# Optimization experiments

Measured on AMD Instinct MI355X. Metric: run time of the kernel, lower is better.

## Reference

```python
import jax, jax.numpy as jnp
import numpy as np

N = 65536       # tokens (voxels)
C = 128         # dim
H = 4           # num_heads
HD = C // H     # head_dim = 32
NUM_WIN = 1024  # number of windows


def setup_inputs() -> dict:
    key = jax.random.key(0)
    k1, k2, k3, k4 = jax.random.split(key, 4)
    x = jax.random.normal(k1, (N, C), dtype=jnp.float32)
    w_qkv = jax.random.normal(k2, (3 * C, C), dtype=jnp.float32) * 0.02
    w_proj = jax.random.normal(k3, (C, C), dtype=jnp.float32) * 0.02
    b_proj = jnp.zeros((C,), dtype=jnp.float32)
    batch_win_inds = jnp.sort(jax.random.randint(k4, (N,), 0, NUM_WIN)).astype(jnp.int32)
    counts = jax.ops.segment_sum(jnp.ones((N,), jnp.int32), batch_win_inds, num_segments=NUM_WIN)
    offsets = jnp.concatenate([jnp.zeros((1,), jnp.int32), jnp.cumsum(counts)]).astype(jnp.int32)
    return {"x": x, "w_qkv": w_qkv, "w_proj": w_proj, "b_proj": b_proj,
            "batch_win_inds": batch_win_inds, "offsets": offsets, "counts": counts}


def reference(x, w_qkv, w_proj, b_proj, batch_win_inds, offsets, counts):
    # qkv projection (no bias), split, per-head reshape
    qkv = (x @ w_qkv.T).reshape(N, 3, H, HD)          # [N,3,H,HD]
    q = jax.nn.relu(qkv[:, 0])                        # [N,H,HD]
    k = jax.nn.relu(qkv[:, 1])                        # [N,H,HD]
    v = qkv[:, 2]                                     # [N,H,HD]

    kv = jax.ops.segment_sum(
        jnp.einsum('nhc,nhd->nhcd', k, v), batch_win_inds, num_segments=NUM_WIN)
    # per-window key sum s[w,h,c]
    s = jax.ops.segment_sum(k, batch_win_inds, num_segments=NUM_WIN)

    y = jnp.einsum('nhc,nhcd->nhd', q, kv[batch_win_inds])
    z = jnp.sum(s[batch_win_inds] * q, axis=-1, keepdims=True)
    y = y / (z + 1e-6)

    y = y.reshape(N, C)
    return y @ w_proj.T + b_proj
```

## Files before the change

kernel.cpp:

```cpp
#include <hip/hip_runtime.h>

namespace {
constexpr int C     = 128;
constexpr int T     = 64;
constexpr int BLK   = 512;
constexpr int NWIN  = 1024;
constexpr int KVSTR = 40;
constexpr int KTSTR = 72;
constexpr int YNSTR = 136;
constexpr int WSPN  = 131072;
constexpr size_t QN = (size_t)65536 * 128;
}

typedef __attribute__((ext_vector_type(8))) short bf16x8;
typedef __attribute__((ext_vector_type(4))) short sh4;
typedef __attribute__((ext_vector_type(4))) float f32x4;

__device__ __forceinline__ short bf16rne(float f) {
    unsigned u = __float_as_uint(f);
    u += 0x7fffu + ((u >> 16) & 1u);
    return (short)(u >> 16);
}
__device__ __forceinline__ float bf16f(short h) {
    return __uint_as_float(((unsigned)(unsigned short)h) << 16);
}
__device__ __forceinline__ void split1(float f, short& hi, short& lo) {
    hi = bf16rne(f);
    lo = bf16rne(f - bf16f(hi));
}

__global__ void prep_weights(const float* __restrict__ wqkv,
                             const float* __restrict__ wproj,
                             short* __restrict__ wsp) {
    const int i = blockIdx.x * 256 + threadIdx.x;
    const float f = (i < 49152) ? wqkv[i] : wproj[i - 49152];
    short hi, lo;
    split1(f, hi, lo);
    wsp[i] = hi;
    wsp[65536 + i] = lo;
}

__global__ __launch_bounds__(BLK, 2)
void qkv_gemm(const float* __restrict__ x,
              const short* __restrict__ wsp,
              short* __restrict__ qws,
              short* __restrict__ kws,
              short* __restrict__ vws)
{
    __shared__ __align__(16) short xh[64 * YNSTR];
    __shared__ __align__(16) short xl[64 * YNSTR];

    const int tid = threadIdx.x;
    const int wv = tid >> 6, ln = tid & 63;
    const int fr = ln & 15, fg = ln >> 4;
    const int r0 = blockIdx.x * 256;

    bf16x8 Bh[3][4], Bl[3][4];
#pragma unroll
    for (int ni = 0; ni < 3; ++ni)
#pragma unroll
        for (int ksi = 0; ksi < 4; ++ksi) {
            const int idx = ((3 * wv + ni) * 16 + fr) * C + ksi * 32 + fg * 8;
            Bh[ni][ksi] = *(const bf16x8*)(wsp + idx);
            Bl[ni][ksi] = *(const bf16x8*)(wsp + 65536 + idx);
        }

    const int trow = tid >> 3;
    const int toff = (tid & 7) << 4;

    for (int ch = 0; ch < 4; ++ch) {
        const int rbase = r0 + ch * 64;
        if (ch) __syncthreads();

#pragma unroll
        for (int it = 0; it < 2; ++it) {
            const int i = tid + it * BLK;
            const int t = i >> 4, c8 = (i & 15) << 3;
            const float* p = x + (size_t)(rbase + t) * C + c8;
            const float4 a = *(const float4*)p;
            const float4 b = *(const float4*)(p + 4);
            const float f[8] = {a.x, a.y, a.z, a.w, b.x, b.y, b.z, b.w};
            bf16x8 hi, lo;
#pragma unroll
            for (int u = 0; u < 8; ++u) { short h_, l_; split1(f[u], h_, l_); hi[u] = h_; lo[u] = l_; }
            *(bf16x8*)(xh + t * YNSTR + c8) = hi;
            *(bf16x8*)(xl + t * YNSTR + c8) = lo;
        }
        __syncthreads();

        f32x4 acc[3][4];
#pragma unroll
        for (int ni = 0; ni < 3; ++ni)
#pragma unroll
            for (int m = 0; m < 4; ++m) acc[ni][m] = f32x4{0.f, 0.f, 0.f, 0.f};

#pragma unroll
        for (int ksi = 0; ksi < 4; ++ksi) {
            const int koff = ksi * 32 + fg * 8;
            bf16x8 ahi[4], alo[4];
#pragma unroll
            for (int m = 0; m < 4; ++m) {
                const int row = m * 16 + fr;
                ahi[m] = *(const bf16x8*)(xh + row * YNSTR + koff);
                alo[m] = *(const bf16x8*)(xl + row * YNSTR + koff);
            }
#pragma unroll
            for (int ni = 0; ni < 3; ++ni)
#pragma unroll
                for (int m = 0; m < 4; ++m) {
                    acc[ni][m] = __builtin_amdgcn_mfma_f32_16x16x32_bf16(ahi[m], Bh[ni][ksi], acc[ni][m], 0, 0, 0);
                    acc[ni][m] = __builtin_amdgcn_mfma_f32_16x16x32_bf16(ahi[m], Bl[ni][ksi], acc[ni][m], 0, 0, 0);
                    acc[ni][m] = __builtin_amdgcn_mfma_f32_16x16x32_bf16(alo[m], Bh[ni][ksi], acc[ni][m], 0, 0, 0);
                }
        }
        __syncthreads();

#pragma unroll
        for (int ni = 0; ni < 3; ++ni) {
            const int ti = 3 * wv + ni;
            const int p = ti >> 3;
            if (p < 2) {
                short* buf = (p == 0) ? xh : xl;
                const int lc = (ti & 7) * 16 + fr;
#pragma unroll
                for (int m = 0; m < 4; ++m)
#pragma unroll
                    for (int e = 0; e < 4; ++e)
                        buf[(m * 16 + fg * 4 + e) * YNSTR + lc] =
                            bf16rne(fmaxf(acc[ni][m][e], 0.f));
            }
        }
        __syncthreads();
        {
            const bf16x8 q0 = *(const bf16x8*)(xh + trow * YNSTR + toff);
            const bf16x8 q1 = *(const bf16x8*)(xh + trow * YNSTR + toff + 8);
            const bf16x8 k0 = *(const bf16x8*)(xl + trow * YNSTR + toff);
            const bf16x8 k1 = *(const bf16x8*)(xl + trow * YNSTR + toff + 8);
            *(bf16x8*)(qws + (size_t)(rbase + trow) * C + toff)     = q0;
            *(bf16x8*)(qws + (size_t)(rbase + trow) * C + toff + 8) = q1;
            *(bf16x8*)(kws + (size_t)(rbase + trow) * C + toff)     = k0;
            *(bf16x8*)(kws + (size_t)(rbase + trow) * C + toff + 8) = k1;
        }
        __syncthreads();

#pragma unroll
        for (int ni = 0; ni < 3; ++ni) {
            const int ti = 3 * wv + ni;
            if ((ti >> 3) == 2) {
                const int lc = (ti & 7) * 16 + fr;
#pragma unroll
                for (int m = 0; m < 4; ++m)
#pragma unroll
                    for (int e = 0; e < 4; ++e)
                        xh[(m * 16 + fg * 4 + e) * YNSTR + lc] = bf16rne(acc[ni][m][e]);
            }
        }
        __syncthreads();
        {
            const bf16x8 v0 = *(const bf16x8*)(xh + trow * YNSTR + toff);
            const bf16x8 v1 = *(const bf16x8*)(xh + trow * YNSTR + toff + 8);
            *(bf16x8*)(vws + (size_t)(rbase + trow) * C + toff)     = v0;
            *(bf16x8*)(vws + (size_t)(rbase + trow) * C + toff + 8) = v1;
        }
    }
}

__global__ __launch_bounds__(BLK, 2)
void sla_win(const short* __restrict__ qws,
             const short* __restrict__ kws,
             const short* __restrict__ vws,
             const short* __restrict__ wsp,
             const float* __restrict__ bproj,
             const int*   __restrict__ offsets,
             float*       __restrict__ out)
{
    __shared__ __align__(16) short kT[C * KTSTR];
    __shared__ __align__(16) short vT[C * KTSTR];
    __shared__ __align__(16) short yn[T * YNSTR];
    __shared__ __align__(16) short kvs[4 * 32 * KVSTR];
    __shared__ float ss[C];

    const int win = blockIdx.x;
    const int beg = offsets[win];
    const int cnt = offsets[win + 1] - beg;
    if (cnt <= 0) return;
    const int nch = (cnt + T - 1) / T;

    const int tid = threadIdx.x;
    const int wv = tid >> 6, ln = tid & 63;
    const int fr = ln & 15, fg = ln >> 4;
    const int aH = wv >> 1, tw = wv & 1;

    f32x4 kvacc[2] = {{0.f,0.f,0.f,0.f},{0.f,0.f,0.f,0.f}};
    f32x4 sacc = {0.f, 0.f, 0.f, 0.f};
    bf16x8 ones;
#pragma unroll
    for (int u = 0; u < 8; ++u) ones[u] = (short)0x3F80;

    for (int c0 = 0; c0 < nch; ++c0) {
        const int t0 = c0 * T;
        const int tc = (cnt - t0 < T) ? (cnt - t0) : T;

#pragma unroll
        for (int it = 0; it < 2; ++it) {
            const int i = tid + it * BLK;
            const int t = i >> 4, c8 = (i & 15) << 3;
            bf16x8 k8, v8;
#pragma unroll
            for (int u = 0; u < 8; ++u) { k8[u] = 0; v8[u] = 0; }
            if (t < tc) {
                k8 = *(const bf16x8*)(kws + (size_t)(beg + t0 + t) * C + c8);
                v8 = *(const bf16x8*)(vws + (size_t)(beg + t0 + t) * C + c8);
            }
#pragma unroll
            for (int u = 0; u < 8; ++u) {
                const int c = c8 + u;
                const int tt = t ^ (((c >> 3) & 7) << 3);
                kT[c * KTSTR + tt] = k8[u];
                vT[c * KTSTR + tt] = v8[u];
            }
        }
        __syncthreads();

        {
#pragma unroll
            for (int kt = 0; kt < 2; ++kt) {
                const int t8 = kt * 32 + fg * 8;
                const int cch = aH * 32 + tw * 16 + fr;
                const bf16x8 a8 = *(const bf16x8*)(kT + cch * KTSTR + (t8 ^ (((cch >> 3) & 7) << 3)));
                sacc = __builtin_amdgcn_mfma_f32_16x16x32_bf16(a8, ones, sacc, 0, 0, 0);
#pragma unroll
                for (int dt = 0; dt < 2; ++dt) {
                    const int dch = aH * 32 + dt * 16 + fr;
                    const bf16x8 b8 = *(const bf16x8*)(vT + dch * KTSTR + (t8 ^ (((dch >> 3) & 7) << 3)));
                    kvacc[dt] = __builtin_amdgcn_mfma_f32_16x16x32_bf16(a8, b8, kvacc[dt], 0, 0, 0);
                }
            }
        }
        if (c0 + 1 < nch) __syncthreads();
    }

    {
#pragma unroll
        for (int dt = 0; dt < 2; ++dt) {
            const int d = dt * 16 + fr;
#pragma unroll
            for (int e = 0; e < 4; ++e) {
                const int c = tw * 16 + fg * 4 + e;
                kvs[aH * (32 * KVSTR) + d * KVSTR + c] = bf16rne(kvacc[dt][e]);
            }
        }
        if (fr == 0) {
#pragma unroll
            for (int e = 0; e < 4; ++e)
                ss[aH * 32 + tw * 16 + fg * 4 + e] = sacc[e];
        }
    }
    __syncthreads();

    for (int c0 = 0; c0 < nch; ++c0) {
        const int t0 = c0 * T;
        const int tc = (cnt - t0 < T) ? (cnt - t0) : T;

        {
            const int a = wv >> 1, mp = wv & 1;
            bf16x8 bfr[2];
#pragma unroll
            for (int dl = 0; dl < 2; ++dl)
                bfr[dl] = *(const bf16x8*)(kvs + a * (32 * KVSTR) + (dl * 16 + fr) * KVSTR + fg * 8);

            const float4 s0 = *(const float4*)(ss + a * 32 + fg * 8);
            const float4 s1 = *(const float4*)(ss + a * 32 + fg * 8 + 4);

            bf16x8 afr[2];
            float zinv[2];
#pragma unroll
            for (int mi = 0; mi < 2; ++mi) {
                const int row = (mp * 2 + mi) * 16 + fr;
                afr[mi] = *(const bf16x8*)(qws + (size_t)(beg + t0 + row) * C + a * 32 + fg * 8);
                float zp = 0.f;
                zp = fmaf(bf16f(afr[mi][0]), s0.x, zp);
                zp = fmaf(bf16f(afr[mi][1]), s0.y, zp);
                zp = fmaf(bf16f(afr[mi][2]), s0.z, zp);
                zp = fmaf(bf16f(afr[mi][3]), s0.w, zp);
                zp = fmaf(bf16f(afr[mi][4]), s1.x, zp);
                zp = fmaf(bf16f(afr[mi][5]), s1.y, zp);
                zp = fmaf(bf16f(afr[mi][6]), s1.z, zp);
                zp = fmaf(bf16f(afr[mi][7]), s1.w, zp);
                zp += __shfl_xor(zp, 16);
                zp += __shfl_xor(zp, 32);
                zinv[mi] = 1.f / (zp + 1e-6f);
            }
            f32x4 acc[2][2];
#pragma unroll
            for (int mi = 0; mi < 2; ++mi)
#pragma unroll
                for (int dl = 0; dl < 2; ++dl) {
                    acc[mi][dl] = f32x4{0.f, 0.f, 0.f, 0.f};
                    acc[mi][dl] = __builtin_amdgcn_mfma_f32_16x16x32_bf16(afr[mi], bfr[dl], acc[mi][dl], 0, 0, 0);
                }
#pragma unroll
            for (int mi = 0; mi < 2; ++mi)
#pragma unroll
                for (int e = 0; e < 4; ++e) {
                    const float zt = __shfl(zinv[mi], fg * 4 + e);
                    const int t = (mp * 2 + mi) * 16 + fg * 4 + e;
#pragma unroll
                    for (int dl = 0; dl < 2; ++dl) {
                        const int ch = a * 32 + dl * 16 + fr;
                        yn[t * YNSTR + ch] = bf16rne(acc[mi][dl][e] * zt);
                    }
                }
        }
        __syncthreads();

        {
            f32x4 acc[4];
#pragma unroll
            for (int m = 0; m < 4; ++m) acc[m] = f32x4{0.f, 0.f, 0.f, 0.f};
#pragma unroll
            for (int ksi = 0; ksi < 4; ++ksi) {
                const int koff = ksi * 32 + fg * 8;
                bf16x8 a8[4];
#pragma unroll
                for (int m = 0; m < 4; ++m) {
                    const int row = m * 16 + fr;
                    a8[m] = *(const bf16x8*)(yn + row * YNSTR + koff);
                }
                const int idx = (384 + wv * 16 + fr) * C + koff;
                const bf16x8 bhi = *(const bf16x8*)(wsp + idx);
                const bf16x8 blo = *(const bf16x8*)(wsp + 65536 + idx);
#pragma unroll
                for (int m = 0; m < 4; ++m) {
                    acc[m] = __builtin_amdgcn_mfma_f32_16x16x32_bf16(a8[m], bhi, acc[m], 0, 0, 0);
                    acc[m] = __builtin_amdgcn_mfma_f32_16x16x32_bf16(a8[m], blo, acc[m], 0, 0, 0);
                }
            }
            const int ch = wv * 16 + fr;
            const float b = bproj[ch];
#pragma unroll
            for (int m = 0; m < 4; ++m)
#pragma unroll
                for (int e = 0; e < 4; ++e) {
                    const int t = m * 16 + fg * 4 + e;
                    if (t < tc)
                        out[(size_t)(beg + t0 + t) * C + ch] = acc[m][e] + b;
                }
        }
        if (c0 + 1 < nch) __syncthreads();
    }
}

__global__ __launch_bounds__(BLK, 2)
void sla6(const float* __restrict__ x, const float* __restrict__ bproj,
          const int* __restrict__ offsets, const short* __restrict__ wsp,
          short* __restrict__ qws, float* __restrict__ out)
{
    __shared__ __align__(16) short xs_hi[T * C];
    __shared__ __align__(16) short xs_lo[T * C];
    __shared__ __align__(16) short kT[C * T];
    __shared__ __align__(16) short vTy[C * T];
    __shared__ __align__(16) short kvs[4 * 32 * KVSTR];
    __shared__ float ss[C];

    const int win = blockIdx.x;
    const int beg = offsets[win];
    const int cnt = offsets[win + 1] - beg;
    if (cnt <= 0) return;
    const int nch = (cnt + T - 1) / T;

    const int tid = threadIdx.x;
    const int wv = tid >> 6, ln = tid & 63;
    const int fr = ln & 15, fg = ln >> 4;

    auto loadB = [&](int row512, int koff, bf16x8& bhi, bf16x8& blo) {
        const int idx = row512 * C + koff;
        bhi = *(const bf16x8*)(wsp + idx);
        blo = *(const bf16x8*)(wsp + 65536 + idx);
    };
    auto stage = [&](int t0, int tc) {
#pragma unroll
        for (int it = 0; it < 2; ++it) {
            const int i = tid + it * BLK;
            const int t = i >> 4, c8 = (i & 15) << 3;
            float4 a = {0.f, 0.f, 0.f, 0.f}, b = {0.f, 0.f, 0.f, 0.f};
            if (t < tc) {
                const float* p = x + (size_t)(beg + t0 + t) * C + c8;
                a = *(const float4*)p;
                b = *(const float4*)(p + 4);
            }
            const float f[8] = {a.x, a.y, a.z, a.w, b.x, b.y, b.z, b.w};
            bf16x8 hi, lo;
#pragma unroll
            for (int u = 0; u < 8; ++u) { short h_, l_; split1(f[u], h_, l_); hi[u] = h_; lo[u] = l_; }
            const int s = t * C + (c8 ^ ((t & 7) << 3));
            *(bf16x8*)(xs_hi + s) = hi;
            *(bf16x8*)(xs_lo + s) = lo;
        }
    };

    const int aH = wv >> 1, tw = wv & 1;
    f32x4 kvacc[2] = {{0.f,0.f,0.f,0.f},{0.f,0.f,0.f,0.f}};
    f32x4 sacc = {0.f, 0.f, 0.f, 0.f};
    bf16x8 ones;
#pragma unroll
    for (int u = 0; u < 8; ++u) ones[u] = (short)0x3F80;

    for (int c0 = 0; c0 < nch; ++c0) {
        const int t0 = c0 * T;
        const int tc = (cnt - t0 < T) ? (cnt - t0) : T;
        stage(t0, tc);
        __syncthreads();
        sh4 qreg[4];
        {
            f32x4 acc[2][4];
#pragma unroll
            for (int ni = 0; ni < 2; ++ni)
#pragma unroll
                for (int m = 0; m < 4; ++m) acc[ni][m] = f32x4{0.f, 0.f, 0.f, 0.f};
#pragma unroll
            for (int ksi = 0; ksi < 4; ++ksi) {
                const int koff = ksi * 32 + fg * 8;
                bf16x8 ahi[4], alo[4];
#pragma unroll
                for (int m = 0; m < 4; ++m) {
                    const int row = m * 16 + fr;
                    const int s = row * C + (koff ^ ((row & 7) << 3));
                    ahi[m] = *(const bf16x8*)(xs_hi + s);
                    alo[m] = *(const bf16x8*)(xs_lo + s);
                }
#pragma unroll
                for (int ni = 0; ni < 2; ++ni) {
                    bf16x8 bhi, blo;
                    loadB(128 + (2 * wv + ni) * 16 + fr, koff, bhi, blo);
#pragma unroll
                    for (int m = 0; m < 4; ++m) {
                        acc[ni][m] = __builtin_amdgcn_mfma_f32_16x16x32_bf16(ahi[m], bhi, acc[ni][m], 0, 0, 0);
                        acc[ni][m] = __builtin_amdgcn_mfma_f32_16x16x32_bf16(ahi[m], blo, acc[ni][m], 0, 0, 0);
                        acc[ni][m] = __builtin_amdgcn_mfma_f32_16x16x32_bf16(alo[m], bhi, acc[ni][m], 0, 0, 0);
                    }
                }
            }
#pragma unroll
            for (int ni = 0; ni < 2; ++ni) {
                const int nt = 2 * wv + ni;
                const bool isk = (nt < 8);
                const int ch = (isk ? nt : nt - 8) * 16 + fr;
                short* dst = isk ? kT : vTy;
#pragma unroll
                for (int m = 0; m < 4; ++m) {
                    sh4 h4;
#pragma unroll
                    for (int e = 0; e < 4; ++e) {
                        float v = acc[ni][m][e];
                        if (isk) v = fmaxf(v, 0.f);
                        h4[e] = bf16rne(v);
                    }
                    const int tb = m * 16 + fg * 4;
                    *(sh4*)(dst + ch * T + (tb ^ ((ch & 7) << 3))) = h4;
                }
            }
        }
        {
            f32x4 acc[4];
#pragma unroll
            for (int m = 0; m < 4; ++m) acc[m] = f32x4{0.f, 0.f, 0.f, 0.f};
#pragma unroll
            for (int ksi = 0; ksi < 4; ++ksi) {
                const int koff = ksi * 32 + fg * 8;
                bf16x8 ahi[4], alo[4];
#pragma unroll
                for (int m = 0; m < 4; ++m) {
                    const int row = m * 16 + fr;
                    const int s = row * C + (koff ^ ((row & 7) << 3));
                    ahi[m] = *(const bf16x8*)(xs_hi + s);
                    alo[m] = *(const bf16x8*)(xs_lo + s);
                }
                bf16x8 bhi, blo;
                loadB(wv * 16 + fr, koff, bhi, blo);
#pragma unroll
                for (int m = 0; m < 4; ++m) {
                    acc[m] = __builtin_amdgcn_mfma_f32_16x16x32_bf16(ahi[m], bhi, acc[m], 0, 0, 0);
                    acc[m] = __builtin_amdgcn_mfma_f32_16x16x32_bf16(ahi[m], blo, acc[m], 0, 0, 0);
                    acc[m] = __builtin_amdgcn_mfma_f32_16x16x32_bf16(alo[m], bhi, acc[m], 0, 0, 0);
                }
            }
#pragma unroll
            for (int m = 0; m < 4; ++m)
#pragma unroll
                for (int e = 0; e < 4; ++e)
                    qreg[m][e] = bf16rne(fmaxf(acc[m][e], 0.f));
        }
        __syncthreads();
        {
            const int ch = wv * 16 + fr;
            if (nch == 1) {
#pragma unroll
                for (int m = 0; m < 4; ++m)
#pragma unroll
                    for (int e = 0; e < 4; ++e) {
                        const int t = m * 16 + fg * 4 + e;
                        xs_hi[t * C + (ch ^ ((t & 7) << 3))] = qreg[m][e];
                    }
            } else {
#pragma unroll
                for (int m = 0; m < 4; ++m)
#pragma unroll
                    for (int e = 0; e < 4; ++e) {
                        const int t = m * 16 + fg * 4 + e;
                        if (t < tc)
                            qws[(size_t)(beg + t0 + t) * C + ch] = qreg[m][e];
                    }
            }
        }
        {
#pragma unroll
            for (int kt = 0; kt < 2; ++kt) {
                const int t8 = kt * 32 + fg * 8;
                const int cch = aH * 32 + tw * 16 + fr;
                const bf16x8 a8 = *(const bf16x8*)(kT + cch * T + (t8 ^ ((cch & 7) << 3)));
                sacc = __builtin_amdgcn_mfma_f32_16x16x32_bf16(a8, ones, sacc, 0, 0, 0);
#pragma unroll
                for (int dt = 0; dt < 2; ++dt) {
                    const int dch = aH * 32 + dt * 16 + fr;
                    const bf16x8 b8 = *(const bf16x8*)(vTy + dch * T + (t8 ^ ((dch & 7) << 3)));
                    kvacc[dt] = __builtin_amdgcn_mfma_f32_16x16x32_bf16(a8, b8, kvacc[dt], 0, 0, 0);
                }
            }
        }
        if (c0 + 1 < nch) __syncthreads();
    }
    {
#pragma unroll
        for (int dt = 0; dt < 2; ++dt) {
            const int d = dt * 16 + fr;
#pragma unroll
            for (int e = 0; e < 4; ++e) {
                const int c = tw * 16 + fg * 4 + e;
                kvs[aH * (32 * KVSTR) + d * KVSTR + c] = bf16rne(kvacc[dt][e]);
            }
        }
        if (fr == 0) {
#pragma unroll
            for (int e = 0; e < 4; ++e)
                ss[aH * 32 + tw * 16 + fg * 4 + e] = sacc[e];
        }
    }
    __syncthreads();
    for (int c0 = 0; c0 < nch; ++c0) {
        const int t0 = c0 * T;
        const int tc = (cnt - t0 < T) ? (cnt - t0) : T;
        {
            const int a = wv >> 1, mp = wv & 1;
            bf16x8 bfr[2];
#pragma unroll
            for (int dl = 0; dl < 2; ++dl)
                bfr[dl] = *(const bf16x8*)(kvs + a * (32 * KVSTR) + (dl * 16 + fr) * KVSTR + fg * 8);
            const float4 s0 = *(const float4*)(ss + a * 32 + fg * 8);
            const float4 s1 = *(const float4*)(ss + a * 32 + fg * 8 + 4);
            bf16x8 afr[2];
            float zinv[2];
#pragma unroll
            for (int mi = 0; mi < 2; ++mi) {
                const int row = (mp * 2 + mi) * 16 + fr;
                if (nch == 1)
                    afr[mi] = *(const bf16x8*)(xs_hi + row * C + ((a * 32 + fg * 8) ^ ((row & 7) << 3)));
                else
                    afr[mi] = *(const bf16x8*)(qws + (size_t)(beg + t0 + row) * C + a * 32 + fg * 8);
                float zp = 0.f;
                zp = fmaf(bf16f(afr[mi][0]), s0.x, zp);
                zp = fmaf(bf16f(afr[mi][1]), s0.y, zp);
                zp = fmaf(bf16f(afr[mi][2]), s0.z, zp);
                zp = fmaf(bf16f(afr[mi][3]), s0.w, zp);
                zp = fmaf(bf16f(afr[mi][4]), s1.x, zp);
                zp = fmaf(bf16f(afr[mi][5]), s1.y, zp);
                zp = fmaf(bf16f(afr[mi][6]), s1.z, zp);
                zp = fmaf(bf16f(afr[mi][7]), s1.w, zp);
                zp += __shfl_xor(zp, 16);
                zp += __shfl_xor(zp, 32);
                zinv[mi] = 1.f / (zp + 1e-6f);
            }
            f32x4 acc[2][2];
#pragma unroll
            for (int mi = 0; mi < 2; ++mi)
#pragma unroll
                for (int dl = 0; dl < 2; ++dl) {
                    acc[mi][dl] = f32x4{0.f, 0.f, 0.f, 0.f};
                    acc[mi][dl] = __builtin_amdgcn_mfma_f32_16x16x32_bf16(afr[mi], bfr[dl], acc[mi][dl], 0, 0, 0);
                }
#pragma unroll
            for (int mi = 0; mi < 2; ++mi)
#pragma unroll
                for (int e = 0; e < 4; ++e) {
                    const float zt = __shfl(zinv[mi], fg * 4 + e);
                    const int t = (mp * 2 + mi) * 16 + fg * 4 + e;
#pragma unroll
                    for (int dl = 0; dl < 2; ++dl) {
                        const int ch = a * 32 + dl * 16 + fr;
                        vTy[t * C + (ch ^ ((t & 7) << 3))] = bf16rne(acc[mi][dl][e] * zt);
                    }
                }
        }
        __syncthreads();
        {
            f32x4 acc[4];
#pragma unroll
            for (int m = 0; m < 4; ++m) acc[m] = f32x4{0.f, 0.f, 0.f, 0.f};
#pragma unroll
            for (int ksi = 0; ksi < 4; ++ksi) {
                const int koff = ksi * 32 + fg * 8;
                bf16x8 a8[4];
#pragma unroll
                for (int m = 0; m < 4; ++m) {
                    const int row = m * 16 + fr;
                    a8[m] = *(const bf16x8*)(vTy + row * C + (koff ^ ((row & 7) << 3)));
                }
                bf16x8 bhi, blo;
                loadB(384 + wv * 16 + fr, koff, bhi, blo);
#pragma unroll
                for (int m = 0; m < 4; ++m) {
                    acc[m] = __builtin_amdgcn_mfma_f32_16x16x32_bf16(a8[m], bhi, acc[m], 0, 0, 0);
                    acc[m] = __builtin_amdgcn_mfma_f32_16x16x32_bf16(a8[m], blo, acc[m], 0, 0, 0);
                }
            }
            const int ch = wv * 16 + fr;
            const float b = bproj[ch];
#pragma unroll
            for (int m = 0; m < 4; ++m)
#pragma unroll
                for (int e = 0; e < 4; ++e) {
                    const int t = m * 16 + fg * 4 + e;
                    if (t < tc)
                        out[(size_t)(beg + t0 + t) * C + ch] = acc[m][e] + b;
                }
        }
        if (c0 + 1 < nch) __syncthreads();
    }
}

extern "C" void kernel_launch(void* const* d_in, const int* in_sizes, int n_in,
                              void* d_out, int out_size, void* d_ws, size_t ws_size,
                              hipStream_t stream)
{
    const float* x       = (const float*)d_in[0];
    const float* wqkv    = (const float*)d_in[1];
    const float* wproj   = (const float*)d_in[2];
    const float* bproj   = (const float*)d_in[3];
    const int*   offsets = (const int*)d_in[5];
    float* out = (float*)d_out;
    short* wsp = (short*)d_ws;

    const size_t need_split = ((size_t)WSPN + 3 * QN) * sizeof(short);
    const size_t need_sla6  = ((size_t)WSPN + QN) * sizeof(short);

    if (ws_size >= need_split) {
        short* qws = wsp + WSPN;
        short* kws = qws + QN;
        short* vws = kws + QN;
        hipLaunchKernelGGL(prep_weights, dim3(256), dim3(256), 0, stream, wqkv, wproj, wsp);
        hipLaunchKernelGGL(qkv_gemm, dim3(65536 / 256), dim3(BLK), 0, stream,
                           x, wsp, qws, kws, vws);
        hipLaunchKernelGGL(sla_win, dim3(NWIN), dim3(BLK), 0, stream,
                           qws, kws, vws, wsp, bproj, offsets, out);
    } else if (ws_size >= need_sla6) {
        hipLaunchKernelGGL(prep_weights, dim3(256), dim3(256), 0, stream, wqkv, wproj, wsp);
        hipLaunchKernelGGL(sla6, dim3(NWIN), dim3(BLK), 0, stream,
                           x, bproj, offsets, wsp, wsp + WSPN, out);
    }
}
```

Baseline: 71.64 us.

## Restructure qkv_gemm: 128-row blocks, prefetch next chunk, separate output staging

The QKV GEMM now handles 128 rows per block in two 64-row chunks instead of 256 rows in four, doubling the grid to 512 blocks. The second chunk of x is loaded into registers while the first chunk's MFMAs run, then split into bf16 hi/lo after compute. Results are staged in new shared buffers (os1/os2) so the input tile is not overwritten, and weight fragments are read from global/L2 inside the k-loop instead of being kept in registers. The aim is more parallelism across CUs and overlap of global loads with compute. The cost is doubled LDS per block, which may lower occupancy, plus repeated weight loads.

```diff
diff --git a/kernel.cpp b/kernel.cpp
--- a/kernel.cpp
+++ b/kernel.cpp
@@ -49,44 +49,44 @@
 {
     __shared__ __align__(16) short xh[64 * YNSTR];
     __shared__ __align__(16) short xl[64 * YNSTR];
+    __shared__ __align__(16) short os1[64 * YNSTR];
+    __shared__ __align__(16) short os2[64 * YNSTR];
 
     const int tid = threadIdx.x;
     const int wv = tid >> 6, ln = tid & 63;
     const int fr = ln & 15, fg = ln >> 4;
-    const int r0 = blockIdx.x * 256;
-
-    bf16x8 Bh[3][4], Bl[3][4];
-#pragma unroll
-    for (int ni = 0; ni < 3; ++ni)
-#pragma unroll
-        for (int ksi = 0; ksi < 4; ++ksi) {
-            const int idx = ((3 * wv + ni) * 16 + fr) * C + ksi * 32 + fg * 8;
-            Bh[ni][ksi] = *(const bf16x8*)(wsp + idx);
-            Bl[ni][ksi] = *(const bf16x8*)(wsp + 65536 + idx);
-        }
-
+    const int r0 = blockIdx.x * 128;
+
+    const int st_t0 = tid >> 4;
+    const int st_c8 = (tid & 15) << 3;
     const int trow = tid >> 3;
     const int toff = (tid & 7) << 4;
 
-    for (int ch = 0; ch < 4; ++ch) {
-        const int rbase = r0 + ch * 64;
-        if (ch) __syncthreads();
-
-#pragma unroll
-        for (int it = 0; it < 2; ++it) {
-            const int i = tid + it * BLK;
-            const int t = i >> 4, c8 = (i & 15) << 3;
-            const float* p = x + (size_t)(rbase + t) * C + c8;
-            const float4 a = *(const float4*)p;
-            const float4 b = *(const float4*)(p + 4);
-            const float f[8] = {a.x, a.y, a.z, a.w, b.x, b.y, b.z, b.w};
-            bf16x8 hi, lo;
-#pragma unroll
-            for (int u = 0; u < 8; ++u) { short h_, l_; split1(f[u], h_, l_); hi[u] = h_; lo[u] = l_; }
-            *(bf16x8*)(xh + t * YNSTR + c8) = hi;
-            *(bf16x8*)(xl + t * YNSTR + c8) = lo;
-        }
-        __syncthreads();
+#pragma unroll
+    for (int it = 0; it < 2; ++it) {
+        const int t = st_t0 + it * 32;
+        const float* p = x + (size_t)(r0 + t) * C + st_c8;
+        const float4 a = *(const float4*)p;
+        const float4 b = *(const float4*)(p + 4);
+        const float f[8] = {a.x, a.y, a.z, a.w, b.x, b.y, b.z, b.w};
+        bf16x8 hi, lo;
+#pragma unroll
+        for (int u = 0; u < 8; ++u) { short h_, l_; split1(f[u], h_, l_); hi[u] = h_; lo[u] = l_; }
+        *(bf16x8*)(xh + t * YNSTR + st_c8) = hi;
+        *(bf16x8*)(xl + t * YNSTR + st_c8) = lo;
+    }
+    float4 xr[4];
+#pragma unroll
+    for (int it = 0; it < 2; ++it) {
+        const int t = st_t0 + it * 32;
+        const float* p = x + (size_t)(r0 + 64 + t) * C + st_c8;
+        xr[2 * it]     = *(const float4*)p;
+        xr[2 * it + 1] = *(const float4*)(p + 4);
+    }
+    __syncthreads();
+
+    for (int c = 0; c < 2; ++c) {
+        const int rbase = r0 + c * 64;
 
         f32x4 acc[3][4];
 #pragma unroll
@@ -105,22 +105,40 @@
                 alo[m] = *(const bf16x8*)(xl + row * YNSTR + koff);
             }
 #pragma unroll
-            for (int ni = 0; ni < 3; ++ni)
-#pragma unroll
-                for (int m = 0; m < 4; ++m) {
-                    acc[ni][m] = __builtin_amdgcn_mfma_f32_16x16x32_bf16(ahi[m], Bh[ni][ksi], acc[ni][m], 0, 0, 0);
-                    acc[ni][m] = __builtin_amdgcn_mfma_f32_16x16x32_bf16(ahi[m], Bl[ni][ksi], acc[ni][m], 0, 0, 0);
-                    acc[ni][m] = __builtin_amdgcn_mfma_f32_16x16x32_bf16(alo[m], Bh[ni][ksi], acc[ni][m], 0, 0, 0);
-                }
-        }
-        __syncthreads();
+            for (int ni = 0; ni < 3; ++ni) {
+                const int idx = ((3 * wv + ni) * 16 + fr) * C + koff;
+                const bf16x8 bhi = *(const bf16x8*)(wsp + idx);
+                const bf16x8 blo = *(const bf16x8*)(wsp + 65536 + idx);
+#pragma unroll
+                for (int m = 0; m < 4; ++m) {
+                    acc[ni][m] = __builtin_amdgcn_mfma_f32_16x16x32_bf16(ahi[m], bhi, acc[ni][m], 0, 0, 0);
+                    acc[ni][m] = __builtin_amdgcn_mfma_f32_16x16x32_bf16(ahi[m], blo, acc[ni][m], 0, 0, 0);
+                    acc[ni][m] = __builtin_amdgcn_mfma_f32_16x16x32_bf16(alo[m], bhi, acc[ni][m], 0, 0, 0);
+                }
+            }
+        }
+        __syncthreads();
+
+        if (c == 0) {
+#pragma unroll
+            for (int it = 0; it < 2; ++it) {
+                const int t = st_t0 + it * 32;
+                const float f[8] = {xr[2 * it].x, xr[2 * it].y, xr[2 * it].z, xr[2 * it].w,
+                                    xr[2 * it + 1].x, xr[2 * it + 1].y, xr[2 * it + 1].z, xr[2 * it + 1].w};
+                bf16x8 hi, lo;
+#pragma unroll
+                for (int u = 0; u < 8; ++u) { short h_, l_; split1(f[u], h_, l_); hi[u] = h_; lo[u] = l_; }
+                *(bf16x8*)(xh + t * YNSTR + st_c8) = hi;
+                *(bf16x8*)(xl + t * YNSTR + st_c8) = lo;
+            }
+        }
 
 #pragma unroll
         for (int ni = 0; ni < 3; ++ni) {
             const int ti = 3 * wv + ni;
             const int p = ti >> 3;
             if (p < 2) {
-                short* buf = (p == 0) ? xh : xl;
+                short* buf = (p == 0) ? os1 : os2;
                 const int lc = (ti & 7) * 16 + fr;
 #pragma unroll
                 for (int m = 0; m < 4; ++m)
@@ -132,10 +150,10 @@
         }
         __syncthreads();
         {
-            const bf16x8 q0 = *(const bf16x8*)(xh + trow * YNSTR + toff);
-            const bf16x8 q1 = *(const bf16x8*)(xh + trow * YNSTR + toff + 8);
-            const bf16x8 k0 = *(const bf16x8*)(xl + trow * YNSTR + toff);
-            const bf16x8 k1 = *(const bf16x8*)(xl + trow * YNSTR + toff + 8);
+            const bf16x8 q0 = *(const bf16x8*)(os1 + trow * YNSTR + toff);
+            const bf16x8 q1 = *(const bf16x8*)(os1 + trow * YNSTR + toff + 8);
+            const bf16x8 k0 = *(const bf16x8*)(os2 + trow * YNSTR + toff);
+            const bf16x8 k1 = *(const bf16x8*)(os2 + trow * YNSTR + toff + 8);
             *(bf16x8*)(qws + (size_t)(rbase + trow) * C + toff)     = q0;
             *(bf16x8*)(qws + (size_t)(rbase + trow) * C + toff + 8) = q1;
             *(bf16x8*)(kws + (size_t)(rbase + trow) * C + toff)     = k0;
@@ -152,13 +170,13 @@
                 for (int m = 0; m < 4; ++m)
 #pragma unroll
                     for (int e = 0; e < 4; ++e)
-                        xh[(m * 16 + fg * 4 + e) * YNSTR + lc] = bf16rne(acc[ni][m][e]);
-            }
-        }
-        __syncthreads();
-        {
-            const bf16x8 v0 = *(const bf16x8*)(xh + trow * YNSTR + toff);
-            const bf16x8 v1 = *(const bf16x8*)(xh + trow * YNSTR + toff + 8);
+                        os1[(m * 16 + fg * 4 + e) * YNSTR + lc] = bf16rne(acc[ni][m][e]);
+            }
+        }
+        __syncthreads();
+        {
+            const bf16x8 v0 = *(const bf16x8*)(os1 + trow * YNSTR + toff);
+            const bf16x8 v1 = *(const bf16x8*)(os1 + trow * YNSTR + toff + 8);
             *(bf16x8*)(vws + (size_t)(rbase + trow) * C + toff)     = v0;
             *(bf16x8*)(vws + (size_t)(rbase + trow) * C + toff + 8) = v1;
         }
@@ -658,7 +676,7 @@
         short* kws = qws + QN;
         short* vws = kws + QN;
         hipLaunchKernelGGL(prep_weights, dim3(256), dim3(256), 0, stream, wqkv, wproj, wsp);
-        hipLaunchKernelGGL(qkv_gemm, dim3(65536 / 256), dim3(BLK), 0, stream,
+        hipLaunchKernelGGL(qkv_gemm, dim3(65536 / 128), dim3(BLK), 0, stream,
                            x, wsp, qws, kws, vws);
         hipLaunchKernelGGL(sla_win, dim3(NWIN), dim3(BLK), 0, stream,
                            qws, kws, vws, wsp, bproj, offsets, out);
```

New measurement: 76.61 us. 6.9% more time.
